# Kernel optimization log

Measured on AMD Instinct MI355X. Metric: run time of the kernel, lower is better.

Reference implementation:

```python
import jax, jax.numpy as jnp
import numpy as np
import math

N_HEADS = 16

def setup_inputs() -> dict:
    key = jax.random.key(0)
    k1, k2, k3 = jax.random.split(key, 3)
    B, S, D = 2, 2048, 1024
    x = jax.random.normal(k1, (B, S, D), dtype=jnp.float32)
    qkv = 0.01 * jax.random.normal(k2, (3 * D, D), dtype=jnp.float32)
    wo = 0.01 * jax.random.normal(k3, (D, D), dtype=jnp.float32)
    return {"x": x, "qkv": qkv, "wo": wo}

def reference(x, qkv, wo):
    B, S, D = x.shape
    H = N_HEADS
    dh = D // H
    QKV = x @ qkv.T                      # [B,S,3D]
    Q, K, V = jnp.split(QKV, 3, axis=-1)
    q = Q.reshape(B, S, H, dh).transpose(0, 2, 1, 3)  # [B,H,S,dh]
    k = K.reshape(B, S, H, dh).transpose(0, 2, 1, 3)
    v = V.reshape(B, S, H, dh).transpose(0, 2, 1, 3)
    scores = jnp.einsum('bhqd,bhkd->bhqk', q, k) / math.sqrt(float(dh))
    # Faithful to original: multiply by lower-triangular mask, then set
    # exact zeros to -inf (masked positions become 0 then -inf).
    mask = jnp.tril(jnp.ones((S, S), dtype=scores.dtype))
    scores = scores * mask[None, None, :, :]
    scores = jnp.where(scores == 0, -jnp.inf, scores)
    attn = jax.nn.softmax(scores, axis=-1)
    out = jnp.einsum('bhqk,bhkd->bhqd', attn, v)       # [B,H,S,dh]
    out = out.transpose(0, 2, 1, 3).reshape(B, S, D)
    return out @ wo.T
```

## Files before the change

kernel.cpp:

```cpp
#include <hip/hip_runtime.h>

typedef unsigned short u16;
typedef unsigned int u32;
typedef __bf16 bf16x8 __attribute__((ext_vector_type(8)));
typedef float f32x4 __attribute__((ext_vector_type(4)));
typedef u16 u16x4 __attribute__((ext_vector_type(4)));

#define GL2LDS16(g, l)                                                         \
    __builtin_amdgcn_global_load_lds(                                          \
        (__attribute__((address_space(1))) const void*)(g),                    \
        (__attribute__((address_space(3))) void*)(l), 16, 0, 0)

#define SYNC_VM(n) asm volatile("s_waitcnt vmcnt(" #n ")\ns_barrier" ::: "memory")
#define BAR()      asm volatile("s_barrier" ::: "memory")

__device__ __forceinline__ u16 f2bf(float f) {
    union { float f; u32 u; } x; x.f = f;
    u32 r = x.u + 0x7FFFu + ((x.u >> 16) & 1u);
    return (u16)(r >> 16);
}

__global__ __launch_bounds__(256) void convert_all_kernel(const float* __restrict__ x,
                                                          const float* __restrict__ qkv,
                                                          const float* __restrict__ wo,
                                                          u16* __restrict__ out) {
    int i = (blockIdx.x * 256 + threadIdx.x) * 4;
    const float* src;
    int off;
    if (i < 4194304)      { src = x;   off = i; }
    else if (i < 7340032) { src = qkv; off = i - 4194304; }
    else                  { src = wo;  off = i - 7340032; }
    float4 v = *(const float4*)(src + off);
    u16x4 o;
    o.x = f2bf(v.x); o.y = f2bf(v.y); o.z = f2bf(v.z); o.w = f2bf(v.w);
    *(u16x4*)(out + i) = o;
}

template <int TM, bool OUT_BF16>
__global__ __launch_bounds__(256) void gemm_bt(const u16* __restrict__ A,
                                               const u16* __restrict__ B,
                                               void* __restrict__ Cout,
                                               int M, int N, int K) {
    constexpr int MI = TM / 32;
    __shared__ u16 As[2][TM * 32];
    __shared__ u16 Bs[2][128 * 32];
    const int tid = threadIdx.x;
    const int w = tid >> 6, lane = tid & 63, ln = lane & 15, qd = lane >> 4;
    const int wr = w >> 1, wc = w & 1;
    const int m0 = blockIdx.y * TM, n0 = blockIdx.x * 128;

    const int srow = tid >> 2, scol = (tid & 3) * 8;
    const u16* Abase = A + (size_t)(m0 + srow) * K + scol;
    const u16* Bbase = B + (size_t)(n0 + srow) * K + scol;

    f32x4 acc[MI][4] = {};
    const int nsteps = K >> 5;

#pragma unroll
    for (int it = 0; it < TM / 64; ++it)
        GL2LDS16(Abase + (size_t)(it * 64) * K, &As[0][(tid + it * 256) * 8]);
#pragma unroll
    for (int it = 0; it < 2; ++it)
        GL2LDS16(Bbase + (size_t)(it * 64) * K, &Bs[0][(tid + it * 256) * 8]);

    for (int s = 0; s < nsteps; ++s) {
        const u16* Ab = As[s & 1];
        const u16* Bb = Bs[s & 1];
        if (s + 1 < nsteps) {
            const int nk = (s + 1) << 5;
            const int nb = (s + 1) & 1;
#pragma unroll
            for (int it = 0; it < TM / 64; ++it)
                GL2LDS16(Abase + (size_t)(it * 64) * K + nk, &As[nb][(tid + it * 256) * 8]);
#pragma unroll
            for (int it = 0; it < 2; ++it)
                GL2LDS16(Bbase + (size_t)(it * 64) * K + nk, &Bs[nb][(tid + it * 256) * 8]);
            if constexpr (TM == 128) SYNC_VM(4); else SYNC_VM(3);
        } else {
            SYNC_VM(0);
        }

        bf16x8 af[MI], bfr[4];
#pragma unroll
        for (int i = 0; i < MI; ++i)
            af[i] = *(const bf16x8*)&Ab[(wr * (TM / 2) + i * 16 + ln) * 32 + qd * 8];
#pragma unroll
        for (int j = 0; j < 4; ++j)
            bfr[j] = *(const bf16x8*)&Bb[(wc * 64 + j * 16 + ln) * 32 + qd * 8];
#pragma unroll
        for (int i = 0; i < MI; ++i)
#pragma unroll
            for (int j = 0; j < 4; ++j)
                acc[i][j] = __builtin_amdgcn_mfma_f32_16x16x32_bf16(af[i], bfr[j], acc[i][j], 0, 0, 0);
        BAR();
    }

#pragma unroll
    for (int i = 0; i < MI; ++i)
#pragma unroll
        for (int j = 0; j < 4; ++j)
#pragma unroll
            for (int r = 0; r < 4; ++r) {
                int row = m0 + wr * (TM / 2) + i * 16 + qd * 4 + r;
                int col = n0 + wc * 64 + j * 16 + ln;
                float v = acc[i][j][r];
                if constexpr (OUT_BF16)
                    ((u16*)Cout)[(size_t)row * N + col] = f2bf(v);
                else
                    ((float*)Cout)[(size_t)row * N + col] = v;
            }
}

__global__ __launch_bounds__(256) void vtrans_kernel(const u16* __restrict__ QKV,
                                                     u16* __restrict__ VtG) {
    __shared__ u16 T[64 * 72];
    const int tid = threadIdx.x;
    const int bh = blockIdx.y;
    const int b = bh >> 4, h = bh & 15;
    const int s0 = blockIdx.x * 64;
#pragma unroll
    for (int it = 0; it < 2; ++it) {
        int idx = it * 256 + tid;
        int sl = idx >> 3, dg = (idx & 7) << 3;
        union { uint4 v; u16 u[8]; } raw;
        raw.v = *(const uint4*)(QKV + (size_t)(b * 2048 + s0 + sl) * 3072 + 2048 + h * 64 + dg);
#pragma unroll
        for (int j = 0; j < 8; ++j) T[(dg + j) * 72 + sl] = raw.u[j];
    }
    __syncthreads();
#pragma unroll
    for (int it = 0; it < 2; ++it) {
        int idx = it * 256 + tid;
        int d = idx >> 3, sg = (idx & 7) << 3;
        *(uint4*)(VtG + ((size_t)(bh * 64 + d)) * 2048 + s0 + sg) = *(uint4*)&T[d * 72 + sg];
    }
}

__global__ __launch_bounds__(256) void attn_kernel(const u16* __restrict__ QKV,
                                                   const u16* __restrict__ VtG,
                                                   u16* __restrict__ AO) {
    __shared__ u16 Ks[2][64 * 64];
    __shared__ u16 Vts[2][64 * 64];
    __shared__ u16 Pls[4][2][16 * 64];

    const int tid = threadIdx.x;
    const int w = tid >> 6, lane = tid & 63, ln = lane & 15, qd = lane >> 4;
    const int b = blockIdx.z, h = blockIdx.y;
    const int qtA = blockIdx.x;
    const int qtB = 31 - qtA;
    const int myqA = qtA * 64 + w * 16 + ln;
    const int myqB = qtB * 64 + w * 16 + ln;
    const int bh = b * 16 + h;
    const int swz = ln & 7;
    const int nch = qtB + 1;

    const int srow = tid >> 3;
    const int sgg = (tid & 7) ^ (srow & 7);
    const u16* ksrc = QKV + (size_t)(b * 2048 + srow) * 3072 + 1024 + h * 64 + sgg * 8;
    const u16* vsrc = VtG + (size_t)(bh * 64 + srow) * 2048 + sgg * 8;

    GL2LDS16(ksrc, &Ks[0][tid * 8]);
    GL2LDS16(ksrc + (size_t)32 * 3072, &Ks[0][tid * 8 + 2048]);
    GL2LDS16(vsrc, &Vts[0][tid * 8]);
    GL2LDS16(vsrc + (size_t)32 * 2048, &Vts[0][tid * 8 + 2048]);

    const u16* qpA = QKV + (size_t)(b * 2048 + myqA) * 3072 + h * 64;
    const u16* qpB = QKV + (size_t)(b * 2048 + myqB) * 3072 + h * 64;
    bf16x8 qfA0 = *(const bf16x8*)(qpA + qd * 8);
    bf16x8 qfA1 = *(const bf16x8*)(qpA + 32 + qd * 8);
    bf16x8 qfB0 = *(const bf16x8*)(qpB + qd * 8);
    bf16x8 qfB1 = *(const bf16x8*)(qpB + 32 + qd * 8);

    f32x4 oA[4] = {}, oB[4] = {};
    float lA = 0.f, lB = 0.f;
    u16* PwA = &Pls[w][0][0];
    u16* PwB = &Pls[w][1][0];

    for (int c = 0; c < nch; ++c) {
        if (c + 1 < nch) {
            const int k1 = (c + 1) * 64;
            const int nb = (c + 1) & 1;
            GL2LDS16(ksrc + (size_t)k1 * 3072, &Ks[nb][tid * 8]);
            GL2LDS16(ksrc + (size_t)(k1 + 32) * 3072, &Ks[nb][tid * 8 + 2048]);
            GL2LDS16(vsrc + k1, &Vts[nb][tid * 8]);
            GL2LDS16(vsrc + k1 + 32 * 2048, &Vts[nb][tid * 8 + 2048]);
            SYNC_VM(4);
        } else {
            SYNC_VM(0);
        }
        const u16* Kb = Ks[c & 1];
        const u16* Vb = Vts[c & 1];
        const bool actA = (c <= qtA);

        f32x4 sA[4], sB[4];
#pragma unroll
        for (int kt = 0; kt < 4; ++kt) {
            const u16* kr = Kb + (kt * 16 + ln) * 64;
            bf16x8 kf0 = *(const bf16x8*)(kr + ((qd ^ swz) * 8));
            bf16x8 kf1 = *(const bf16x8*)(kr + (((qd + 4) ^ swz) * 8));
            f32x4 z = {0.f, 0.f, 0.f, 0.f};
            z = __builtin_amdgcn_mfma_f32_16x16x32_bf16(kf0, qfB0, z, 0, 0, 0);
            z = __builtin_amdgcn_mfma_f32_16x16x32_bf16(kf1, qfB1, z, 0, 0, 0);
            sB[kt] = z;
            if (actA) {
                f32x4 y = {0.f, 0.f, 0.f, 0.f};
                y = __builtin_amdgcn_mfma_f32_16x16x32_bf16(kf0, qfA0, y, 0, 0, 0);
                y = __builtin_amdgcn_mfma_f32_16x16x32_bf16(kf1, qfA1, y, 0, 0, 0);
                sA[kt] = y;
            }
        }

        if (c == qtB) {
#pragma unroll
            for (int kt = 0; kt < 4; ++kt)
#pragma unroll
                for (int r = 0; r < 4; ++r) {
                    int key = c * 64 + kt * 16 + qd * 4 + r;
                    float v = sB[kt][r] * 0.125f;
                    sB[kt][r] = (key > myqB) ? -1e30f : v;
                }
        } else {
#pragma unroll
            for (int kt = 0; kt < 4; ++kt)
#pragma unroll
                for (int r = 0; r < 4; ++r) sB[kt][r] *= 0.125f;
        }
#pragma unroll
        for (int kt = 0; kt < 4; ++kt) {
            u16x4 pk;
            float p0 = __expf(sB[kt][0]), p1 = __expf(sB[kt][1]);
            float p2 = __expf(sB[kt][2]), p3 = __expf(sB[kt][3]);
            lB += p0 + p1 + p2 + p3;
            pk.x = f2bf(p0); pk.y = f2bf(p1); pk.z = f2bf(p2); pk.w = f2bf(p3);
            int g = kt * 2 + (qd >> 1);
            *(u16x4*)&PwB[ln * 64 + ((g ^ swz) * 8) + (qd & 1) * 4] = pk;
        }
        bf16x8 pfB0 = *(const bf16x8*)&PwB[ln * 64 + ((qd ^ swz) * 8)];
        bf16x8 pfB1 = *(const bf16x8*)&PwB[ln * 64 + (((qd + 4) ^ swz) * 8)];

        bf16x8 pfA0, pfA1;
        if (actA) {
            if (c == qtA) {
#pragma unroll
                for (int kt = 0; kt < 4; ++kt)
#pragma unroll
                    for (int r = 0; r < 4; ++r) {
                        int key = c * 64 + kt * 16 + qd * 4 + r;
                        float v = sA[kt][r] * 0.125f;
                        sA[kt][r] = (key > myqA) ? -1e30f : v;
                    }
            } else {
#pragma unroll
                for (int kt = 0; kt < 4; ++kt)
#pragma unroll
                    for (int r = 0; r < 4; ++r) sA[kt][r] *= 0.125f;
            }
#pragma unroll
            for (int kt = 0; kt < 4; ++kt) {
                u16x4 pk;
                float p0 = __expf(sA[kt][0]), p1 = __expf(sA[kt][1]);
                float p2 = __expf(sA[kt][2]), p3 = __expf(sA[kt][3]);
                lA += p0 + p1 + p2 + p3;
                pk.x = f2bf(p0); pk.y = f2bf(p1); pk.z = f2bf(p2); pk.w = f2bf(p3);
                int g = kt * 2 + (qd >> 1);
                *(u16x4*)&PwA[ln * 64 + ((g ^ swz) * 8) + (qd & 1) * 4] = pk;
            }
            pfA0 = *(const bf16x8*)&PwA[ln * 64 + ((qd ^ swz) * 8)];
            pfA1 = *(const bf16x8*)&PwA[ln * 64 + (((qd + 4) ^ swz) * 8)];
        }

#pragma unroll
        for (int dt = 0; dt < 4; ++dt) {
            const u16* vr = Vb + (dt * 16 + ln) * 64;
            bf16x8 vf0 = *(const bf16x8*)(vr + ((qd ^ swz) * 8));
            bf16x8 vf1 = *(const bf16x8*)(vr + (((qd + 4) ^ swz) * 8));
            oB[dt] = __builtin_amdgcn_mfma_f32_16x16x32_bf16(vf0, pfB0, oB[dt], 0, 0, 0);
            oB[dt] = __builtin_amdgcn_mfma_f32_16x16x32_bf16(vf1, pfB1, oB[dt], 0, 0, 0);
            if (actA) {
                oA[dt] = __builtin_amdgcn_mfma_f32_16x16x32_bf16(vf0, pfA0, oA[dt], 0, 0, 0);
                oA[dt] = __builtin_amdgcn_mfma_f32_16x16x32_bf16(vf1, pfA1, oA[dt], 0, 0, 0);
            }
        }
        BAR();
    }

    lA += __shfl_xor(lA, 16); lA += __shfl_xor(lA, 32);
    lB += __shfl_xor(lB, 16); lB += __shfl_xor(lB, 32);
    float invA = 1.0f / lA, invB = 1.0f / lB;
#pragma unroll
    for (int dt = 0; dt < 4; ++dt) {
        u16x4 ov;
        ov.x = f2bf(oA[dt][0] * invA); ov.y = f2bf(oA[dt][1] * invA);
        ov.z = f2bf(oA[dt][2] * invA); ov.w = f2bf(oA[dt][3] * invA);
        *(u16x4*)&AO[(size_t)(b * 2048 + myqA) * 1024 + h * 64 + dt * 16 + qd * 4] = ov;
        ov.x = f2bf(oB[dt][0] * invB); ov.y = f2bf(oB[dt][1] * invB);
        ov.z = f2bf(oB[dt][2] * invB); ov.w = f2bf(oB[dt][3] * invB);
        *(u16x4*)&AO[(size_t)(b * 2048 + myqB) * 1024 + h * 64 + dt * 16 + qd * 4] = ov;
    }
}

extern "C" void kernel_launch(void* const* d_in, const int* in_sizes, int n_in,
                              void* d_out, int out_size, void* d_ws, size_t ws_size,
                              hipStream_t stream) {
    const float* x   = (const float*)d_in[0];
    const float* qkv = (const float*)d_in[1];
    const float* wo  = (const float*)d_in[2];
    float* out = (float*)d_out;

    char* ws = (char*)d_ws;
    u16* xb   = (u16*)(ws + 0);
    u16* qkvb = (u16*)(ws + 8388608);
    u16* wob  = (u16*)(ws + 14680064);
    u16* QKVo = (u16*)(ws + 16777216);
    u16* AO   = (u16*)(ws + 41943040);
    u16* VtG  = (u16*)(ws + 0);

    convert_all_kernel<<<8192, 256, 0, stream>>>(x, qkv, wo, xb);

    gemm_bt<128, true><<<dim3(24, 32), 256, 0, stream>>>(xb, qkvb, QKVo, 4096, 3072, 1024);

    vtrans_kernel<<<dim3(32, 32), 256, 0, stream>>>(QKVo, VtG);

    attn_kernel<<<dim3(16, 16, 2), 256, 0, stream>>>(QKVo, VtG, AO);

    gemm_bt<64, false><<<dim3(8, 64), 256, 0, stream>>>(AO, wob, out, 4096, 1024, 1024);
}
```

Measured before the change: 192.7 us.

## Split attention into 32-row query tiles with 2 waves and fold scale into Q

Attention blocks now use 128 threads covering 32-query tiles, with the causal pairing going from 16 to 32 blocks per head and doubling the grid. That gives finer load balance and more resident blocks. The 1/sqrt(d)·log2(e) scale is folded into Q fragments once, so the per-score multiply goes away and exp2 replaces __expf. bf16 packing switches to a cheaper perm-based round-half-up, and P staging shares one LDS buffer per wave. The risks are extra K/V loads per query row, since each block streams the full key range for fewer queries, plus a small change in rounding.

```diff
diff --git a/kernel.cpp b/kernel.cpp
--- a/kernel.cpp
+++ b/kernel.cpp
@@ -18,6 +18,18 @@
     union { float f; u32 u; } x; x.f = f;
     u32 r = x.u + 0x7FFFu + ((x.u >> 16) & 1u);
     return (u16)(r >> 16);
+}
+
+__device__ __forceinline__ u32 pack2bf(float f0, float f1) {
+    union { float f; u32 u; } a, b;
+    a.f = f0; b.f = f1;
+    return __builtin_amdgcn_perm(b.u + 0x8000u, a.u + 0x8000u, 0x07060302u);
+}
+
+__device__ __forceinline__ bf16x8 scale_frag(bf16x8 v) {
+#pragma unroll
+    for (int i = 0; i < 8; ++i) v[i] = (__bf16)((float)v[i] * 0.1803368801f);
+    return v;
 }
 
 __global__ __launch_bounds__(256) void convert_all_kernel(const float* __restrict__ x,
@@ -136,61 +148,63 @@
     }
 }
 
-__global__ __launch_bounds__(256) void attn_kernel(const u16* __restrict__ QKV,
+__global__ __launch_bounds__(128) void attn_kernel(const u16* __restrict__ QKV,
                                                    const u16* __restrict__ VtG,
                                                    u16* __restrict__ AO) {
     __shared__ u16 Ks[2][64 * 64];
     __shared__ u16 Vts[2][64 * 64];
-    __shared__ u16 Pls[4][2][16 * 64];
+    __shared__ u16 Pls[2][16 * 64];
 
     const int tid = threadIdx.x;
     const int w = tid >> 6, lane = tid & 63, ln = lane & 15, qd = lane >> 4;
     const int b = blockIdx.z, h = blockIdx.y;
     const int qtA = blockIdx.x;
-    const int qtB = 31 - qtA;
-    const int myqA = qtA * 64 + w * 16 + ln;
-    const int myqB = qtB * 64 + w * 16 + ln;
+    const int qtB = 63 - qtA;
+    const int XA = qtA * 32 + w * 16;
+    const int XB = qtB * 32 + w * 16;
+    const int myqA = XA + ln, myqB = XB + ln;
     const int bh = b * 16 + h;
     const int swz = ln & 7;
-    const int nch = qtB + 1;
-
-    const int srow = tid >> 3;
-    const int sgg = (tid & 7) ^ (srow & 7);
-    const u16* ksrc = QKV + (size_t)(b * 2048 + srow) * 3072 + 1024 + h * 64 + sgg * 8;
-    const u16* vsrc = VtG + (size_t)(bh * 64 + srow) * 2048 + sgg * 8;
-
-    GL2LDS16(ksrc, &Ks[0][tid * 8]);
-    GL2LDS16(ksrc + (size_t)32 * 3072, &Ks[0][tid * 8 + 2048]);
-    GL2LDS16(vsrc, &Vts[0][tid * 8]);
-    GL2LDS16(vsrc + (size_t)32 * 2048, &Vts[0][tid * 8 + 2048]);
+    const int nch = (qtB >> 1) + 1;
+
+    const int sr0 = tid >> 3;
+    const int sg = (tid & 7) ^ (sr0 & 7);
+    const u16* ksrc = QKV + (size_t)(b * 2048 + sr0) * 3072 + 1024 + h * 64 + sg * 8;
+    const u16* vsrc = VtG + (size_t)(bh * 64 + sr0) * 2048 + sg * 8;
+
+#pragma unroll
+    for (int i = 0; i < 4; ++i) {
+        GL2LDS16(ksrc + (size_t)(i * 16) * 3072, &Ks[0][(i * 128 + tid) * 8]);
+        GL2LDS16(vsrc + (size_t)(i * 16) * 2048, &Vts[0][(i * 128 + tid) * 8]);
+    }
 
     const u16* qpA = QKV + (size_t)(b * 2048 + myqA) * 3072 + h * 64;
     const u16* qpB = QKV + (size_t)(b * 2048 + myqB) * 3072 + h * 64;
-    bf16x8 qfA0 = *(const bf16x8*)(qpA + qd * 8);
-    bf16x8 qfA1 = *(const bf16x8*)(qpA + 32 + qd * 8);
-    bf16x8 qfB0 = *(const bf16x8*)(qpB + qd * 8);
-    bf16x8 qfB1 = *(const bf16x8*)(qpB + 32 + qd * 8);
+    bf16x8 qfA0 = scale_frag(*(const bf16x8*)(qpA + qd * 8));
+    bf16x8 qfA1 = scale_frag(*(const bf16x8*)(qpA + 32 + qd * 8));
+    bf16x8 qfB0 = scale_frag(*(const bf16x8*)(qpB + qd * 8));
+    bf16x8 qfB1 = scale_frag(*(const bf16x8*)(qpB + 32 + qd * 8));
 
     f32x4 oA[4] = {}, oB[4] = {};
     float lA = 0.f, lB = 0.f;
-    u16* PwA = &Pls[w][0][0];
-    u16* PwB = &Pls[w][1][0];
+    u16* Pw = Pls[w];
 
     for (int c = 0; c < nch; ++c) {
         if (c + 1 < nch) {
             const int k1 = (c + 1) * 64;
             const int nb = (c + 1) & 1;
-            GL2LDS16(ksrc + (size_t)k1 * 3072, &Ks[nb][tid * 8]);
-            GL2LDS16(ksrc + (size_t)(k1 + 32) * 3072, &Ks[nb][tid * 8 + 2048]);
-            GL2LDS16(vsrc + k1, &Vts[nb][tid * 8]);
-            GL2LDS16(vsrc + k1 + 32 * 2048, &Vts[nb][tid * 8 + 2048]);
-            SYNC_VM(4);
+#pragma unroll
+            for (int i = 0; i < 4; ++i) {
+                GL2LDS16(ksrc + (size_t)(k1 + i * 16) * 3072, &Ks[nb][(i * 128 + tid) * 8]);
+                GL2LDS16(vsrc + (size_t)(i * 16) * 2048 + k1, &Vts[nb][(i * 128 + tid) * 8]);
+            }
+            SYNC_VM(8);
         } else {
             SYNC_VM(0);
         }
         const u16* Kb = Ks[c & 1];
         const u16* Vb = Vts[c & 1];
-        const bool actA = (c <= qtA);
+        const bool actA = (c * 64 <= XA + 15);
 
         f32x4 sA[4], sB[4];
 #pragma unroll
@@ -210,63 +224,49 @@
             }
         }
 
-        if (c == qtB) {
+        if (c * 64 + 63 > XB) {
 #pragma unroll
             for (int kt = 0; kt < 4; ++kt)
 #pragma unroll
                 for (int r = 0; r < 4; ++r) {
                     int key = c * 64 + kt * 16 + qd * 4 + r;
-                    float v = sB[kt][r] * 0.125f;
-                    sB[kt][r] = (key > myqB) ? -1e30f : v;
+                    if (key > myqB) sB[kt][r] = -1e30f;
                 }
-        } else {
-#pragma unroll
-            for (int kt = 0; kt < 4; ++kt)
-#pragma unroll
-                for (int r = 0; r < 4; ++r) sB[kt][r] *= 0.125f;
         }
 #pragma unroll
         for (int kt = 0; kt < 4; ++kt) {
-            u16x4 pk;
-            float p0 = __expf(sB[kt][0]), p1 = __expf(sB[kt][1]);
-            float p2 = __expf(sB[kt][2]), p3 = __expf(sB[kt][3]);
-            lB += p0 + p1 + p2 + p3;
-            pk.x = f2bf(p0); pk.y = f2bf(p1); pk.z = f2bf(p2); pk.w = f2bf(p3);
+            float p0 = exp2f(sB[kt][0]), p1 = exp2f(sB[kt][1]);
+            float p2 = exp2f(sB[kt][2]), p3 = exp2f(sB[kt][3]);
+            lB += (p0 + p1) + (p2 + p3);
+            uint2 pk = {pack2bf(p0, p1), pack2bf(p2, p3)};
             int g = kt * 2 + (qd >> 1);
-            *(u16x4*)&PwB[ln * 64 + ((g ^ swz) * 8) + (qd & 1) * 4] = pk;
-        }
-        bf16x8 pfB0 = *(const bf16x8*)&PwB[ln * 64 + ((qd ^ swz) * 8)];
-        bf16x8 pfB1 = *(const bf16x8*)&PwB[ln * 64 + (((qd + 4) ^ swz) * 8)];
+            *(uint2*)&Pw[ln * 64 + ((g ^ swz) * 8) + (qd & 1) * 4] = pk;
+        }
+        bf16x8 pfB0 = *(const bf16x8*)&Pw[ln * 64 + ((qd ^ swz) * 8)];
+        bf16x8 pfB1 = *(const bf16x8*)&Pw[ln * 64 + (((qd + 4) ^ swz) * 8)];
 
         bf16x8 pfA0, pfA1;
         if (actA) {
-            if (c == qtA) {
+            if (c * 64 + 63 > XA) {
 #pragma unroll
                 for (int kt = 0; kt < 4; ++kt)
 #pragma unroll
                     for (int r = 0; r < 4; ++r) {
                         int key = c * 64 + kt * 16 + qd * 4 + r;
-                        float v = sA[kt][r] * 0.125f;
-                        sA[kt][r] = (key > myqA) ? -1e30f : v;
+                        if (key > myqA) sA[kt][r] = -1e30f;
                     }
-            } else {
-#pragma unroll
-                for (int kt = 0; kt < 4; ++kt)
-#pragma unroll
-                    for (int r = 0; r < 4; ++r) sA[kt][r] *= 0.125f;
             }
 #pragma unroll
             for (int kt = 0; kt < 4; ++kt) {
-                u16x4 pk;
-                float p0 = __expf(sA[kt][0]), p1 = __expf(sA[kt][1]);
-                float p2 = __expf(sA[kt][2]), p3 = __expf(sA[kt][3]);
-                lA += p0 + p1 + p2 + p3;
-                pk.x = f2bf(p0); pk.y = f2bf(p1); pk.z = f2bf(p2); pk.w = f2bf(p3);
+                float p0 = exp2f(sA[kt][0]), p1 = exp2f(sA[kt][1]);
+                float p2 = exp2f(sA[kt][2]), p3 = exp2f(sA[kt][3]);
+                lA += (p0 + p1) + (p2 + p3);
+                uint2 pk = {pack2bf(p0, p1), pack2bf(p2, p3)};
                 int g = kt * 2 + (qd >> 1);
-                *(u16x4*)&PwA[ln * 64 + ((g ^ swz) * 8) + (qd & 1) * 4] = pk;
-            }
-            pfA0 = *(const bf16x8*)&PwA[ln * 64 + ((qd ^ swz) * 8)];
-            pfA1 = *(const bf16x8*)&PwA[ln * 64 + (((qd + 4) ^ swz) * 8)];
+                *(uint2*)&Pw[ln * 64 + ((g ^ swz) * 8) + (qd & 1) * 4] = pk;
+            }
+            pfA0 = *(const bf16x8*)&Pw[ln * 64 + ((qd ^ swz) * 8)];
+            pfA1 = *(const bf16x8*)&Pw[ln * 64 + (((qd + 4) ^ swz) * 8)];
         }
 
 #pragma unroll
@@ -289,13 +289,12 @@
     float invA = 1.0f / lA, invB = 1.0f / lB;
 #pragma unroll
     for (int dt = 0; dt < 4; ++dt) {
-        u16x4 ov;
-        ov.x = f2bf(oA[dt][0] * invA); ov.y = f2bf(oA[dt][1] * invA);
-        ov.z = f2bf(oA[dt][2] * invA); ov.w = f2bf(oA[dt][3] * invA);
-        *(u16x4*)&AO[(size_t)(b * 2048 + myqA) * 1024 + h * 64 + dt * 16 + qd * 4] = ov;
-        ov.x = f2bf(oB[dt][0] * invB); ov.y = f2bf(oB[dt][1] * invB);
-        ov.z = f2bf(oB[dt][2] * invB); ov.w = f2bf(oB[dt][3] * invB);
-        *(u16x4*)&AO[(size_t)(b * 2048 + myqB) * 1024 + h * 64 + dt * 16 + qd * 4] = ov;
+        uint2 ovA = {pack2bf(oA[dt][0] * invA, oA[dt][1] * invA),
+                     pack2bf(oA[dt][2] * invA, oA[dt][3] * invA)};
+        *(uint2*)&AO[(size_t)(b * 2048 + myqA) * 1024 + h * 64 + dt * 16 + qd * 4] = ovA;
+        uint2 ovB = {pack2bf(oB[dt][0] * invB, oB[dt][1] * invB),
+                     pack2bf(oB[dt][2] * invB, oB[dt][3] * invB)};
+        *(uint2*)&AO[(size_t)(b * 2048 + myqB) * 1024 + h * 64 + dt * 16 + qd * 4] = ovB;
     }
 }
 
@@ -321,7 +320,7 @@
 
     vtrans_kernel<<<dim3(32, 32), 256, 0, stream>>>(QKVo, VtG);
 
-    attn_kernel<<<dim3(16, 16, 2), 256, 0, stream>>>(QKVo, VtG, AO);
+    attn_kernel<<<dim3(32, 16, 2), 128, 0, stream>>>(QKVo, VtG, AO);
 
     gemm_bt<64, false><<<dim3(8, 64), 256, 0, stream>>>(AO, wob, out, 4096, 1024, 1024);
 }
```

Measured after the change: 202.7 us. 5.2% more time.
